# Kernel optimization log

Measured on AMD Instinct MI355X. Metric: run time of the kernel, lower is better.

The kernel has to match this reference:

```python
import jax, jax.numpy as jnp
import numpy as np

B, T, K = 128, 4096, 64
START, STOP = 62, 63
NEG = -10000.0


def setup_inputs() -> dict:
    key = jax.random.key(0)
    k1, k2, k3 = jax.random.split(key, 3)
    feats = jax.random.normal(k1, (B, T, K), dtype=jnp.float32)
    # gold tags never include START/STOP
    tags = jax.random.randint(k2, (B, T), 0, START)
    transitions = jax.random.normal(k3, (K, K), dtype=jnp.float32)
    # mirror the torch __init__ masking: no transition INTO start, none OUT of stop
    transitions = transitions.at[START, :].set(NEG).at[:, STOP].set(NEG)
    return {"feats": feats, "tags": tags, "transitions": transitions}


def _crf_single(feats, tags, transitions):
    """feats: [T,K], tags: [T], transitions: [K,K] (trans[next, prev])."""
    init = jnp.full((K,), NEG, dtype=feats.dtype).at[START].set(0.0)

    # ---- forward algorithm (log partition), vectorized over the tag loop ----
    def fwd_step(alpha, feat):
        # alpha[i] + trans[j, i] + feat[j]  ->  logsumexp over prev i
        new = jax.nn.logsumexp(alpha[None, :] + transitions, axis=1) + feat
        return new, None

    alpha, _ = jax.lax.scan(fwd_step, init, feats)
    forward_score = jax.nn.logsumexp(alpha + transitions[STOP])

    # ---- gold path score (_score_session) ----
    prev_tags = jnp.concatenate([jnp.array([START], dtype=tags.dtype), tags[:-1]])
    emit = jnp.take_along_axis(feats, tags[:, None], axis=1)[:, 0]  # feats[t, tags[t]]
    gold_score = jnp.sum(transitions[tags, prev_tags] + emit) + transitions[STOP, tags[-1]]

    nll = forward_score - gold_score  # neg_log_likelihood

    # ---- Viterbi decode ----
    def vit_step(delta, feat):
        scores = delta[None, :] + transitions  # [next, prev]
        bp = jnp.argmax(scores, axis=1)
        new = jnp.max(scores, axis=1) + feat  # feat added after argmax, as in torch
        return new, bp

    delta, bps = jax.lax.scan(vit_step, init, feats)  # bps: [T, K]
    terminal = delta + transitions[STOP]
    best_last = jnp.argmax(terminal)
    path_score = terminal[best_last]

    def back_step(tag, bp_t):
        return bp_t[tag], tag

    _, best_path = jax.lax.scan(back_step, best_last, bps, reverse=True)  # [T]
    return nll, path_score, best_path


def reference(feats, tags, transitions):
    nll, path_score, best_path = jax.vmap(_crf_single, in_axes=(0, 0, None))(
        feats, tags, transitions
    )
    return nll, path_score, best_path
```

## Files before the change

### kernel.cpp

```cpp
#include <hip/hip_runtime.h>

namespace {
constexpr int Tn = 4096;
constexpr int Kn = 64;
constexpr int BATCH = 128;
constexpr int START_TAG = 62;
constexpr int STOP_TAG = 63;
constexpr float NEGV = -10000.0f;
constexpr int CH = 64;
constexpr int NCH = Tn / CH;
constexpr int GL = 8;
constexpr int NG = Tn / GL;
constexpr int WV = 4;
constexpr int SL = Kn / WV;
constexpr int KP = 66;

__device__ __forceinline__ float rfl(float x) {
    return __uint_as_float(__builtin_amdgcn_readfirstlane(__float_as_uint(x)));
}
__device__ __forceinline__ void bar() {
    __asm__ volatile("s_waitcnt lgkmcnt(0)\n\ts_barrier" ::: "memory");
}
__device__ __forceinline__ void vmdrain() {
    __asm__ volatile("s_waitcnt vmcnt(0)" ::: "memory");
}
__device__ __forceinline__ unsigned int fkey(float x) {
    unsigned int b = __float_as_uint(x);
    return (b & 0x80000000u) ? ~b : (b | 0x80000000u);
}
__device__ __forceinline__ float unkey(unsigned int hb) {
    return __uint_as_float((hb & 0x80000000u) ? (hb ^ 0x80000000u) : ~hb);
}

__global__ __launch_bounds__(256)
void crf_kernel(const float* __restrict__ feats,
                const int* __restrict__ tags,
                const float* __restrict__ trans,
                float* __restrict__ out,
                unsigned int* __restrict__ bp32)
{
    const int tid = threadIdx.x;
    const int lane = tid & 63;
    const int wid = tid >> 6;
    const int b = blockIdx.x & (BATCH - 1);
    const size_t fb = (size_t)b * Tn * Kn;

    __shared__ float pvs[WV][2][Kn];
    __shared__ float wp[2][WV * KP];
    __shared__ float dvs[WV][2][Kn];
    __shared__ unsigned long long kp[2][WV * KP];
    __shared__ float gw[WV];
    __shared__ unsigned char snap[NCH * Kn];
    __shared__ unsigned char echain[NCH];

    if (blockIdx.x < BATCH) {
        float gold = 0.0f;
        {
            const int t0 = tid * (Tn / 256);
            int prev = (tid == 0) ? START_TAG : tags[(size_t)b * Tn + t0 - 1];
            for (int k = 0; k < Tn / 256; ++k) {
                const int t = t0 + k;
                const int tg = tags[(size_t)b * Tn + t];
                gold += trans[tg * Kn + prev] + feats[fb + (size_t)t * Kn + tg];
                prev = tg;
            }
            if (tid == 255) gold += trans[STOP_TAG * Kn + prev];
            #pragma unroll
            for (int off = 32; off; off >>= 1) gold += __shfl_down(gold, off);
            if (lane == 0) gw[wid] = gold;
        }
        float ES[SL];
        #pragma unroll
        for (int q = 0; q < SL / 4; ++q) {
            const float4 t4 = ((const float4*)(trans + lane * Kn + wid * SL))[q];
            ES[4*q+0] = __expf(t4.x); ES[4*q+1] = __expf(t4.y);
            ES[4*q+2] = __expf(t4.z); ES[4*q+3] = __expf(t4.w);
        }
        pvs[wid][0][lane] = (lane == START_TAG) ? 1.0f : 0.0f;
        float O = 0.0f, v = 0.0f;

        float fc[GL], fn[GL], Fc[GL];
        #pragma unroll
        for (int k = 0; k < GL; ++k) fc[k] = feats[fb + (size_t)k * Kn + lane];
        bar();
        for (int g = 0; g < NG; ++g) {
            if (g + 1 < NG) {
                const size_t base = fb + (size_t)(g + 1) * GL * Kn + lane;
                #pragma unroll
                for (int k = 0; k < GL; ++k) fn[k] = feats[base + (size_t)k * Kn];
            }
            #pragma unroll
            for (int k = 0; k < GL; ++k) Fc[k] = __expf(fc[k]);
            #pragma unroll
            for (int k = 0; k < GL; ++k) {
                const int t = g * GL + k;
                const int p = t & 1;
                const float4* vp = (const float4*)&pvs[wid][p][wid * SL];
                const float4 v0 = vp[0], v1 = vp[1], v2 = vp[2], v3 = vp[3];
                float s0 = 0.f, s1 = 0.f, s2 = 0.f, s3 = 0.f;
                s0 = fmaf(ES[0],  v0.x, s0); s1 = fmaf(ES[1],  v0.y, s1);
                s2 = fmaf(ES[2],  v0.z, s2); s3 = fmaf(ES[3],  v0.w, s3);
                s0 = fmaf(ES[4],  v1.x, s0); s1 = fmaf(ES[5],  v1.y, s1);
                s2 = fmaf(ES[6],  v1.z, s2); s3 = fmaf(ES[7],  v1.w, s3);
                s0 = fmaf(ES[8],  v2.x, s0); s1 = fmaf(ES[9],  v2.y, s1);
                s2 = fmaf(ES[10], v2.z, s2); s3 = fmaf(ES[11], v2.w, s3);
                s0 = fmaf(ES[12], v3.x, s0); s1 = fmaf(ES[13], v3.y, s1);
                s2 = fmaf(ES[14], v3.z, s2); s3 = fmaf(ES[15], v3.w, s3);
                wp[p][wid * KP + lane] = (s0 + s1) + (s2 + s3);
                bar();
                const float w0r = wp[p][0 * KP + lane];
                const float w1r = wp[p][1 * KP + lane];
                const float w2r = wp[p][2 * KP + lane];
                const float w3r = wp[p][3 * KP + lane];
                const float w = ((w0r + w1r) + (w2r + w3r)) * Fc[k];
                const float wz = rfl(w);
                O += __logf(wz);
                v = w * __builtin_amdgcn_rcpf(wz);
                pvs[wid][p ^ 1][lane] = v;
            }
            #pragma unroll
            for (int k = 0; k < GL; ++k) fc[k] = fn[k];
        }
        if (wid == 0) {
            const float a = O + __logf(v);
            const float x = a + trans[STOP_TAG * Kn + lane];
            float mx = x;
            #pragma unroll
            for (int off = 32; off; off >>= 1) mx = fmaxf(mx, __shfl_xor(mx, off));
            float se = __expf(x - mx);
            #pragma unroll
            for (int off = 32; off; off >>= 1) se += __shfl_xor(se, off);
            if (lane == 0)
                out[b] = (mx + __logf(se)) - (((gw[0] + gw[1]) + (gw[2] + gw[3])));
        }
    } else {
        float trS[SL];
        #pragma unroll
        for (int q = 0; q < SL / 4; ++q) {
            const float4 t4 = ((const float4*)(trans + lane * Kn + wid * SL))[q];
            trS[4*q+0] = t4.x; trS[4*q+1] = t4.y;
            trS[4*q+2] = t4.z; trS[4*q+3] = t4.w;
        }
        dvs[wid][0][lane] = (lane == START_TAG) ? 0.0f : NEGV;
        float d = 0.0f;
        int h = lane;
        unsigned int bp4 = 0;
        const size_t dwb = (size_t)b * (Tn / 4);

        float fc[GL], fn[GL];
        #pragma unroll
        for (int k = 0; k < GL; ++k) fc[k] = feats[fb + (size_t)k * Kn + lane];
        bar();
        for (int g = 0; g < NG; ++g) {
            if (g + 1 < NG) {
                const size_t base = fb + (size_t)(g + 1) * GL * Kn + lane;
                #pragma unroll
                for (int k = 0; k < GL; ++k) fn[k] = feats[base + (size_t)k * Kn];
            }
            #pragma unroll
            for (int k = 0; k < GL; ++k) {
                const int t = g * GL + k;
                const int p = t & 1;
                const float4* dp = (const float4*)&dvs[wid][p][wid * SL];
                float gv[4]; int gi[4];
                #pragma unroll
                for (int q = 0; q < 4; ++q) {
                    const float4 dv = dp[q];
                    const int i0 = wid * SL + 4 * q;
                    const float sx = dv.x + trS[4*q+0];
                    const float sy = dv.y + trS[4*q+1];
                    const float sz = dv.z + trS[4*q+2];
                    const float sw = dv.w + trS[4*q+3];
                    const bool c01 = sy > sx;
                    const float v01 = c01 ? sy : sx; const int i01 = c01 ? i0+1 : i0;
                    const bool c23 = sw > sz;
                    const float v23 = c23 ? sw : sz; const int i23 = c23 ? i0+3 : i0+2;
                    const bool cq = v23 > v01;
                    gv[q] = cq ? v23 : v01; gi[q] = cq ? i23 : i01;
                }
                const bool ca = gv[1] > gv[0];
                const float va = ca ? gv[1] : gv[0]; const int ia = ca ? gi[1] : gi[0];
                const bool cb = gv[3] > gv[2];
                const float vb = cb ? gv[3] : gv[2]; const int ib = cb ? gi[3] : gi[2];
                const bool cm = vb > va;
                const float m = cm ? vb : va; const int li = cm ? ib : ia;
                kp[p][wid * KP + lane] =
                    ((unsigned long long)fkey(m) << 32) | (unsigned long long)(63 - li);
                bar();
                const unsigned long long k0 = kp[p][0 * KP + lane];
                const unsigned long long k1 = kp[p][1 * KP + lane];
                const unsigned long long k2 = kp[p][2 * KP + lane];
                const unsigned long long k3 = kp[p][3 * KP + lane];
                const unsigned long long ka = k0 > k1 ? k0 : k1;
                const unsigned long long kb = k2 > k3 ? k2 : k3;
                const unsigned long long km = ka > kb ? ka : kb;
                const int bp = 63 - (int)(unsigned int)(km & 0xffffffffULL);
                d = unkey((unsigned int)(km >> 32)) + fc[k];
                dvs[wid][p ^ 1][lane] = d;
                if (wid == 3) {
                    if ((k & 3) == 0) bp4 = (unsigned int)bp;
                    else bp4 |= (unsigned int)bp << (8 * (k & 3));
                    if ((k & 3) == 3)
                        bp32[(dwb + (size_t)(2 * g + (k >> 2))) * Kn + lane] = bp4;
                    h = __shfl(h, bp);
                    if ((t & (CH - 1)) == (CH - 1)) {
                        snap[(t >> 6) * Kn + lane] = (unsigned char)h;
                        h = lane;
                    }
                }
            }
            #pragma unroll
            for (int k = 0; k < GL; ++k) fc[k] = fn[k];
        }
        vmdrain();
        if (wid == 3) {
            const float term = d + trans[STOP_TAG * Kn + lane];
            float bv = term;
            int bi = lane;
            #pragma unroll
            for (int off = 32; off; off >>= 1) {
                const float ov = __shfl_xor(bv, off);
                const int oi = __shfl_xor(bi, off);
                if (ov > bv || (ov == bv && oi < bi)) { bv = ov; bi = oi; }
            }
            if (lane == 0) {
                out[BATCH + b] = bv;
                int e = bi;
                for (int c = NCH - 1; c >= 0; --c) {
                    echain[c] = (unsigned char)e;
                    e = snap[c * Kn + e];
                }
            }
        }
        bar();
        if (wid == 0) {
            int tag = echain[lane];
            float* po = out + 2 * BATCH + (size_t)b * Tn;
            for (int k = CH - 1; k >= 0; --k) {
                const int t = lane * CH + k;
                po[t] = (float)tag;
                tag = (int)((bp32[(dwb + (size_t)(t >> 2)) * Kn + tag] >> (8 * (t & 3))) & 63u);
            }
        }
    }
}
}

extern "C" void kernel_launch(void* const* d_in, const int* in_sizes, int n_in,
                              void* d_out, int out_size, void* d_ws, size_t ws_size,
                              hipStream_t stream)
{
    const float* feats = (const float*)d_in[0];
    const int* tags   = (const int*)d_in[1];
    const float* trans = (const float*)d_in[2];
    float* out = (float*)d_out;
    unsigned int* bp = (unsigned int*)d_ws;
    hipLaunchKernelGGL(crf_kernel, dim3(2 * BATCH), dim3(256), 0, stream,
                       feats, tags, trans, out, bp);
}
```

Baseline: 1.649 ms.

## Run CRF recurrences in single wavefronts with producer-consumer wave pipeline for Viterbi

```diff
diff --git a/kernel.cpp b/kernel.cpp
--- a/kernel.cpp
+++ b/kernel.cpp
@@ -11,33 +11,22 @@
 constexpr int NCH = Tn / CH;
 constexpr int GL = 8;
 constexpr int NG = Tn / GL;
-constexpr int WV = 4;
-constexpr int SL = Kn / WV;
-constexpr int KP = 66;
+constexpr int RS = 32;
+constexpr int RB = 128;
 
 __device__ __forceinline__ float rfl(float x) {
     return __uint_as_float(__builtin_amdgcn_readfirstlane(__float_as_uint(x)));
 }
-__device__ __forceinline__ void bar() {
-    __asm__ volatile("s_waitcnt lgkmcnt(0)\n\ts_barrier" ::: "memory");
-}
-__device__ __forceinline__ void vmdrain() {
-    __asm__ volatile("s_waitcnt vmcnt(0)" ::: "memory");
-}
-__device__ __forceinline__ unsigned int fkey(float x) {
-    unsigned int b = __float_as_uint(x);
-    return (b & 0x80000000u) ? ~b : (b | 0x80000000u);
-}
-__device__ __forceinline__ float unkey(unsigned int hb) {
-    return __uint_as_float((hb & 0x80000000u) ? (hb ^ 0x80000000u) : ~hb);
-}
-
-__global__ __launch_bounds__(256)
+__device__ __forceinline__ void cfence() { __asm__ volatile("" ::: "memory"); }
+__device__ __forceinline__ void lgkm0() { __asm__ volatile("s_waitcnt lgkmcnt(0)" ::: "memory"); }
+__device__ __forceinline__ int imin(int a, int b) { return a < b ? a : b; }
+
+__global__ __launch_bounds__(256, 1)
 void crf_kernel(const float* __restrict__ feats,
                 const int* __restrict__ tags,
                 const float* __restrict__ trans,
                 float* __restrict__ out,
-                unsigned int* __restrict__ bp32)
+                unsigned char* __restrict__ bp8)
 {
     const int tid = threadIdx.x;
     const int lane = tid & 63;
@@ -45,13 +34,15 @@
     const int b = blockIdx.x & (BATCH - 1);
     const size_t fb = (size_t)b * Tn * Kn;
 
-    __shared__ float pvs[WV][2][Kn];
-    __shared__ float wp[2][WV * KP];
-    __shared__ float dvs[WV][2][Kn];
-    __shared__ unsigned long long kp[2][WV * KP];
-    __shared__ float gw[WV];
+    __shared__ float gw[4];
+    __shared__ __align__(16) float vbuf[Kn];
+    __shared__ __align__(16) float ring_v[RS][Kn];
+    __shared__ float ring_m[RS][Kn];
+    __shared__ unsigned char ring_bp[RB][Kn];
     __shared__ unsigned char snap[NCH * Kn];
     __shared__ unsigned char echain[NCH];
+    __shared__ int prog_a[Kn], prog_b[Kn], prog_c[Kn], prog_d[Kn];
+    __shared__ int done_b[Kn], done_c[Kn];
 
     if (blockIdx.x < BATCH) {
         float gold = 0.0f;
@@ -69,20 +60,21 @@
             for (int off = 32; off; off >>= 1) gold += __shfl_down(gold, off);
             if (lane == 0) gw[wid] = gold;
         }
-        float ES[SL];
-        #pragma unroll
-        for (int q = 0; q < SL / 4; ++q) {
-            const float4 t4 = ((const float4*)(trans + lane * Kn + wid * SL))[q];
+        __syncthreads();
+        if (wid != 0) return;
+
+        float ES[Kn];
+        #pragma unroll
+        for (int q = 0; q < Kn / 4; ++q) {
+            const float4 t4 = ((const float4*)(trans + lane * Kn))[q];
             ES[4*q+0] = __expf(t4.x); ES[4*q+1] = __expf(t4.y);
             ES[4*q+2] = __expf(t4.z); ES[4*q+3] = __expf(t4.w);
         }
-        pvs[wid][0][lane] = (lane == START_TAG) ? 1.0f : 0.0f;
-        float O = 0.0f, v = 0.0f;
-
+        float v = (lane == START_TAG) ? 1.0f : 0.0f;
+        float O = 0.0f;
         float fc[GL], fn[GL], Fc[GL];
         #pragma unroll
         for (int k = 0; k < GL; ++k) fc[k] = feats[fb + (size_t)k * Kn + lane];
-        bar();
         for (int g = 0; g < NG; ++g) {
             if (g + 1 < NG) {
                 const size_t base = fb + (size_t)(g + 1) * GL * Kn + lane;
@@ -93,35 +85,34 @@
             for (int k = 0; k < GL; ++k) Fc[k] = __expf(fc[k]);
             #pragma unroll
             for (int k = 0; k < GL; ++k) {
-                const int t = g * GL + k;
-                const int p = t & 1;
-                const float4* vp = (const float4*)&pvs[wid][p][wid * SL];
-                const float4 v0 = vp[0], v1 = vp[1], v2 = vp[2], v3 = vp[3];
-                float s0 = 0.f, s1 = 0.f, s2 = 0.f, s3 = 0.f;
-                s0 = fmaf(ES[0],  v0.x, s0); s1 = fmaf(ES[1],  v0.y, s1);
-                s2 = fmaf(ES[2],  v0.z, s2); s3 = fmaf(ES[3],  v0.w, s3);
-                s0 = fmaf(ES[4],  v1.x, s0); s1 = fmaf(ES[5],  v1.y, s1);
-                s2 = fmaf(ES[6],  v1.z, s2); s3 = fmaf(ES[7],  v1.w, s3);
-                s0 = fmaf(ES[8],  v2.x, s0); s1 = fmaf(ES[9],  v2.y, s1);
-                s2 = fmaf(ES[10], v2.z, s2); s3 = fmaf(ES[11], v2.w, s3);
-                s0 = fmaf(ES[12], v3.x, s0); s1 = fmaf(ES[13], v3.y, s1);
-                s2 = fmaf(ES[14], v3.z, s2); s3 = fmaf(ES[15], v3.w, s3);
-                wp[p][wid * KP + lane] = (s0 + s1) + (s2 + s3);
-                bar();
-                const float w0r = wp[p][0 * KP + lane];
-                const float w1r = wp[p][1 * KP + lane];
-                const float w2r = wp[p][2 * KP + lane];
-                const float w3r = wp[p][3 * KP + lane];
-                const float w = ((w0r + w1r) + (w2r + w3r)) * Fc[k];
+                vbuf[lane] = v;
+                lgkm0();
+                const float4* vp = (const float4*)vbuf;
+                float wq[4];
+                #pragma unroll
+                for (int q = 0; q < 4; ++q) {
+                    const float4 v0 = vp[4*q+0], v1 = vp[4*q+1],
+                                 v2 = vp[4*q+2], v3 = vp[4*q+3];
+                    float s0 = 0.f, s1 = 0.f, s2 = 0.f, s3 = 0.f;
+                    s0 = fmaf(ES[16*q+0],  v0.x, s0); s1 = fmaf(ES[16*q+1],  v0.y, s1);
+                    s2 = fmaf(ES[16*q+2],  v0.z, s2); s3 = fmaf(ES[16*q+3],  v0.w, s3);
+                    s0 = fmaf(ES[16*q+4],  v1.x, s0); s1 = fmaf(ES[16*q+5],  v1.y, s1);
+                    s2 = fmaf(ES[16*q+6],  v1.z, s2); s3 = fmaf(ES[16*q+7],  v1.w, s3);
+                    s0 = fmaf(ES[16*q+8],  v2.x, s0); s1 = fmaf(ES[16*q+9],  v2.y, s1);
+                    s2 = fmaf(ES[16*q+10], v2.z, s2); s3 = fmaf(ES[16*q+11], v2.w, s3);
+                    s0 = fmaf(ES[16*q+12], v3.x, s0); s1 = fmaf(ES[16*q+13], v3.y, s1);
+                    s2 = fmaf(ES[16*q+14], v3.z, s2); s3 = fmaf(ES[16*q+15], v3.w, s3);
+                    wq[q] = (s0 + s1) + (s2 + s3);
+                }
+                const float w = ((wq[0] + wq[1]) + (wq[2] + wq[3])) * Fc[k];
                 const float wz = rfl(w);
                 O += __logf(wz);
                 v = w * __builtin_amdgcn_rcpf(wz);
-                pvs[wid][p ^ 1][lane] = v;
             }
             #pragma unroll
             for (int k = 0; k < GL; ++k) fc[k] = fn[k];
         }
-        if (wid == 0) {
+        {
             const float a = O + __logf(v);
             const float x = a + trans[STOP_TAG * Kn + lane];
             float mx = x;
@@ -133,114 +124,159 @@
             if (lane == 0)
                 out[b] = (mx + __logf(se)) - (((gw[0] + gw[1]) + (gw[2] + gw[3])));
         }
-    } else {
-        float trS[SL];
-        #pragma unroll
-        for (int q = 0; q < SL / 4; ++q) {
-            const float4 t4 = ((const float4*)(trans + lane * Kn + wid * SL))[q];
-            trS[4*q+0] = t4.x; trS[4*q+1] = t4.y;
-            trS[4*q+2] = t4.z; trS[4*q+3] = t4.w;
-        }
-        dvs[wid][0][lane] = (lane == START_TAG) ? 0.0f : NEGV;
-        float d = 0.0f;
-        int h = lane;
-        unsigned int bp4 = 0;
-        const size_t dwb = (size_t)b * (Tn / 4);
-
+        return;
+    }
+
+    volatile int* pa = (volatile int*)prog_a;
+    volatile int* pb = (volatile int*)prog_b;
+    volatile int* pc = (volatile int*)prog_c;
+    volatile int* pd = (volatile int*)prog_d;
+    volatile int* db = (volatile int*)done_b;
+    volatile int* dc = (volatile int*)done_c;
+    if (wid == 0) { pa[lane] = 0; pb[lane] = 0; }
+    if (wid == 1) { pc[lane] = 0; pd[lane] = 0; }
+    if (wid == 2) { db[lane] = 0; dc[lane] = 0; }
+    __syncthreads();
+
+    float trS[Kn];
+    #pragma unroll
+    for (int q = 0; q < Kn / 4; ++q) {
+        const float4 t4 = ((const float4*)(trans + lane * Kn))[q];
+        trS[4*q+0] = t4.x; trS[4*q+1] = t4.y; trS[4*q+2] = t4.z; trS[4*q+3] = t4.w;
+    }
+
+    if (wid == 0) {
+        float v = (lane == START_TAG) ? 0.0f : NEGV;
         float fc[GL], fn[GL];
         #pragma unroll
         for (int k = 0; k < GL; ++k) fc[k] = feats[fb + (size_t)k * Kn + lane];
-        bar();
         for (int g = 0; g < NG; ++g) {
             if (g + 1 < NG) {
                 const size_t base = fb + (size_t)(g + 1) * GL * Kn + lane;
                 #pragma unroll
                 for (int k = 0; k < GL; ++k) fn[k] = feats[base + (size_t)k * Kn];
             }
+            const int tg0 = g * GL;
+            if ((tg0 & 15) == 0 && tg0 >= RS) {
+                cfence();
+                while (pb[lane] < tg0 - 16 || pc[lane] < tg0 - 16) {}
+                cfence();
+            }
             #pragma unroll
             for (int k = 0; k < GL; ++k) {
-                const int t = g * GL + k;
-                const int p = t & 1;
-                const float4* dp = (const float4*)&dvs[wid][p][wid * SL];
-                float gv[4]; int gi[4];
-                #pragma unroll
-                for (int q = 0; q < 4; ++q) {
-                    const float4 dv = dp[q];
-                    const int i0 = wid * SL + 4 * q;
+                const int t = tg0 + k;
+                const int slot = t & (RS - 1);
+                ring_v[slot][lane] = v;
+                lgkm0();
+                const float4* vp = (const float4*)ring_v[slot];
+                float qm[16];
+                #pragma unroll
+                for (int q = 0; q < 16; ++q) {
+                    const float4 dv = vp[q];
                     const float sx = dv.x + trS[4*q+0];
                     const float sy = dv.y + trS[4*q+1];
                     const float sz = dv.z + trS[4*q+2];
                     const float sw = dv.w + trS[4*q+3];
-                    const bool c01 = sy > sx;
-                    const float v01 = c01 ? sy : sx; const int i01 = c01 ? i0+1 : i0;
-                    const bool c23 = sw > sz;
-                    const float v23 = c23 ? sw : sz; const int i23 = c23 ? i0+3 : i0+2;
-                    const bool cq = v23 > v01;
-                    gv[q] = cq ? v23 : v01; gi[q] = cq ? i23 : i01;
+                    qm[q] = fmaxf(fmaxf(sx, sy), fmaxf(sz, sw));
                 }
-                const bool ca = gv[1] > gv[0];
-                const float va = ca ? gv[1] : gv[0]; const int ia = ca ? gi[1] : gi[0];
-                const bool cb = gv[3] > gv[2];
-                const float vb = cb ? gv[3] : gv[2]; const int ib = cb ? gi[3] : gi[2];
-                const bool cm = vb > va;
-                const float m = cm ? vb : va; const int li = cm ? ib : ia;
-                kp[p][wid * KP + lane] =
-                    ((unsigned long long)fkey(m) << 32) | (unsigned long long)(63 - li);
-                bar();
-                const unsigned long long k0 = kp[p][0 * KP + lane];
-                const unsigned long long k1 = kp[p][1 * KP + lane];
-                const unsigned long long k2 = kp[p][2 * KP + lane];
-                const unsigned long long k3 = kp[p][3 * KP + lane];
-                const unsigned long long ka = k0 > k1 ? k0 : k1;
-                const unsigned long long kb = k2 > k3 ? k2 : k3;
-                const unsigned long long km = ka > kb ? ka : kb;
-                const int bp = 63 - (int)(unsigned int)(km & 0xffffffffULL);
-                d = unkey((unsigned int)(km >> 32)) + fc[k];
-                dvs[wid][p ^ 1][lane] = d;
-                if (wid == 3) {
-                    if ((k & 3) == 0) bp4 = (unsigned int)bp;
-                    else bp4 |= (unsigned int)bp << (8 * (k & 3));
-                    if ((k & 3) == 3)
-                        bp32[(dwb + (size_t)(2 * g + (k >> 2))) * Kn + lane] = bp4;
-                    h = __shfl(h, bp);
-                    if ((t & (CH - 1)) == (CH - 1)) {
-                        snap[(t >> 6) * Kn + lane] = (unsigned char)h;
-                        h = lane;
-                    }
-                }
+                float m8[8];
+                #pragma unroll
+                for (int q = 0; q < 8; ++q) m8[q] = fmaxf(qm[2*q], qm[2*q+1]);
+                const float m4a = fmaxf(m8[0], m8[1]), m4b = fmaxf(m8[2], m8[3]);
+                const float m4c = fmaxf(m8[4], m8[5]), m4d = fmaxf(m8[6], m8[7]);
+                const float mm = fmaxf(fmaxf(m4a, m4b), fmaxf(m4c, m4d));
+                ring_m[slot][lane] = mm;
+                cfence();
+                pa[lane] = t + 1;
+                v = mm + fc[k];
             }
             #pragma unroll
             for (int k = 0; k < GL; ++k) fc[k] = fn[k];
         }
-        vmdrain();
-        if (wid == 3) {
-            const float term = d + trans[STOP_TAG * Kn + lane];
-            float bv = term;
-            int bi = lane;
-            #pragma unroll
-            for (int off = 32; off; off >>= 1) {
-                const float ov = __shfl_xor(bv, off);
-                const int oi = __shfl_xor(bi, off);
-                if (ov > bv || (ov == bv && oi < bi)) { bv = ov; bi = oi; }
-            }
-            if (lane == 0) {
-                out[BATCH + b] = bv;
-                int e = bi;
-                for (int c = NCH - 1; c >= 0; --c) {
-                    echain[c] = (unsigned char)e;
-                    e = snap[c * Kn + e];
-                }
-            }
-        }
-        bar();
-        if (wid == 0) {
-            int tag = echain[lane];
-            float* po = out + 2 * BATCH + (size_t)b * Tn;
-            for (int k = CH - 1; k >= 0; --k) {
-                const int t = lane * CH + k;
-                po[t] = (float)tag;
-                tag = (int)((bp32[(dwb + (size_t)(t >> 2)) * Kn + tag] >> (8 * (t & 3))) & 63u);
-            }
+        const float term = v + trans[STOP_TAG * Kn + lane];
+        float bv = term;
+        int bi = lane;
+        #pragma unroll
+        for (int off = 32; off; off >>= 1) {
+            const float ov = __shfl_xor(bv, off);
+            const int oi = __shfl_xor(bi, off);
+            if (ov > bv || (ov == bv && oi < bi)) { bv = ov; bi = oi; }
+        }
+        if (lane == 0) out[BATCH + b] = bv;
+        while (pd[lane] < Tn) __builtin_amdgcn_s_sleep(1);
+        cfence();
+        if (lane == 0) {
+            int e = bi;
+            for (int c = NCH - 1; c >= 0; --c) {
+                echain[c] = (unsigned char)e;
+                e = snap[c * Kn + e];
+            }
+        }
+        lgkm0();
+        while (db[lane] == 0 || dc[lane] == 0) __builtin_amdgcn_s_sleep(1);
+        cfence();
+        int tag = echain[lane];
+        float* po = out + 2 * BATCH + (size_t)b * Tn;
+        const size_t bb = (size_t)b * Tn;
+        for (int k = CH - 1; k >= 0; --k) {
+            const int t = lane * CH + k;
+            po[t] = (float)tag;
+            tag = (int)bp8[(bb + (size_t)t) * Kn + tag];
+        }
+    } else if (wid == 1 || wid == 2) {
+        const int par = wid - 1;
+        const size_t bb = (size_t)b * Tn;
+        volatile int* my = (par == 0) ? pb : pc;
+        for (int t = par; t < Tn; t += 2) {
+            const int slot = t & (RS - 1);
+            while (pa[lane] < t + 1) __builtin_amdgcn_s_sleep(1);
+            cfence();
+            if ((t & 31) == par && t >= RB) {
+                while (pd[lane] < t - 96) __builtin_amdgcn_s_sleep(1);
+                cfence();
+            }
+            const float m = ring_m[slot][lane];
+            const float4* vp = (const float4*)ring_v[slot];
+            int qi[16];
+            #pragma unroll
+            for (int q = 0; q < 16; ++q) {
+                const float4 dv = vp[q];
+                const float sx = dv.x + trS[4*q+0];
+                const float sy = dv.y + trS[4*q+1];
+                const float sz = dv.z + trS[4*q+2];
+                const float sw = dv.w + trS[4*q+3];
+                const int ix = (sx == m) ? 4*q+0 : 255;
+                const int iy = (sy == m) ? 4*q+1 : 255;
+                const int iz = (sz == m) ? 4*q+2 : 255;
+                const int iw = (sw == m) ? 4*q+3 : 255;
+                qi[q] = imin(imin(ix, iy), imin(iz, iw));
+            }
+            int i8[8];
+            #pragma unroll
+            for (int q = 0; q < 8; ++q) i8[q] = imin(qi[2*q], qi[2*q+1]);
+            const int idx = imin(imin(imin(i8[0], i8[1]), imin(i8[2], i8[3])),
+                                 imin(imin(i8[4], i8[5]), imin(i8[6], i8[7])));
+            ring_bp[t & (RB - 1)][lane] = (unsigned char)idx;
+            cfence();
+            my[lane] = t + 1;
+            bp8[(bb + (size_t)t) * Kn + lane] = (unsigned char)idx;
+        }
+        __asm__ volatile("s_waitcnt vmcnt(0)" ::: "memory");
+        if (par == 0) db[lane] = 1; else dc[lane] = 1;
+    } else {
+        int h = lane;
+        for (int t = 0; t < Tn; ++t) {
+            volatile int* pp = (t & 1) ? pc : pb;
+            while (pp[lane] < t + 1) __builtin_amdgcn_s_sleep(1);
+            cfence();
+            const int bp = ring_bp[t & (RB - 1)][lane];
+            h = __shfl(h, bp);
+            if ((t & (CH - 1)) == (CH - 1)) {
+                snap[(t >> 6) * Kn + lane] = (unsigned char)h;
+                h = lane;
+            }
+            cfence();
+            pd[lane] = t + 1;
         }
     }
 }
@@ -254,7 +290,7 @@
     const int* tags   = (const int*)d_in[1];
     const float* trans = (const float*)d_in[2];
     float* out = (float*)d_out;
-    unsigned int* bp = (unsigned int*)d_ws;
+    unsigned char* bp = (unsigned char*)d_ws;
     hipLaunchKernelGGL(crf_kernel, dim3(2 * BATCH), dim3(256), 0, stream,
                        feats, tags, trans, out, bp);
 }
```

New measurement: 2.081 ms. 1.26x slower.
